# Kernel tuning notes

Hardware: AMD Instinct MI355X
Metric: run time of the kernel (lower is better)

Reference implementation:

```python
import jax, jax.numpy as jnp
import numpy as np

# Algorithm constants (scaled-down but structure-identical to the source:
# original Nxy=2304, Nz=300, ItN=60, ROISize=300, NxyExt=128, BkgMean=110, SNR=200)
ItN = 2
BkgMean = 110.0
ROISize = 256
SNR = 200.0
NxyExt = 64
Nxy = 1024
Nz = 24
LO = Nxy // 2 - ROISize   # ROI start inside the padded FFT plane
HI = Nxy // 2 + ROISize   # ROI end


def setup_inputs() -> dict:
    key = jax.random.key(0)
    k1, k2, k3, k4 = jax.random.split(key, 4)
    # raw camera image; uniform in [0, 400) so that subtracting BkgMean=110 keeps signal
    imstack = jax.random.uniform(k1, (1, 1, Nxy - 2 * NxyExt, Nxy - 2 * NxyExt), dtype=jnp.float32) * 400.0
    # initial object volume estimate (the `init` ctor arg)
    init_vol = jax.random.uniform(k2, (1, Nz, 2 * ROISize, 2 * ROISize), dtype=jnp.float32)
    # learned frequency-domain PSF kernel (rand * 0.001, as in __init__)
    conv_real = jax.random.uniform(k3, (1, 1, Nxy, Nxy), dtype=jnp.float32) * 0.001
    conv_imag = jax.random.uniform(k4, (1, 1, Nxy, Nxy), dtype=jnp.float32) * 0.001
    return {"imstack": imstack, "init_vol": init_vol, "conv_real": conv_real, "conv_imag": conv_imag}


def reference(imstack, init_vol, conv_real, conv_imag):
    # Complex frequency-domain kernel; constant across iterations (the source
    # rebuilds/casts it every slice -- same math, hoisted here).
    K = (conv_real + 1j * conv_imag)[0, 0]            # [Nxy, Nxy] complex
    Ksum = jnp.sum(conv_real)

    img = jnp.maximum(imstack - BkgMean, 0.0)
    ImgExp = jnp.pad(img, ((0, 0), (0, 0), (NxyExt, NxyExt), (NxyExt, NxyExt)))  # [1,1,Nxy,Nxy]

    obj = init_vol                                     # [1, Nz, 2R, 2R]
    for _ in range(ItN):
        # --- forward projection: batched over all Nz slices (source loops) ---
        # each slice is placed into the center ROI of a zero [Nxy,Nxy] plane
        vol = jnp.pad(obj, ((0, 0), (0, 0), (LO, Nxy - HI), (LO, Nxy - HI)))  # [1,Nz,Nxy,Nxy]
        est = jnp.real(jnp.fft.ifft2(jnp.fft.fft2(vol) * K)) / Ksum
        ImgEst = jnp.sum(jnp.maximum(est, 0.0), axis=1, keepdims=True)        # [1,1,Nxy,Nxy]

        # --- ratio image (interior only; border stays 1) ---
        Tmp = jnp.median(ImgEst)
        inner = ImgExp[:, :, NxyExt:-NxyExt, NxyExt:-NxyExt] / (
            ImgEst[:, :, NxyExt:-NxyExt, NxyExt:-NxyExt] + Tmp / SNR)
        Ratio = jnp.ones((1, 1, Nxy, Nxy), dtype=ImgEst.dtype)
        Ratio = Ratio.at[:, :, NxyExt:-NxyExt, NxyExt:-NxyExt].set(inner)

        # --- back projection: in the source, fft2(Ratio)*conj(K) is identical for
        # every jj (Ratio and K do not change inside the loop), so compute once ---
        back = jnp.real(jnp.fft.ifft2(jnp.fft.fft2(Ratio) * jnp.conj(K))) / Ksum
        back = jnp.maximum(back, 0.0)                  # [1,1,Nxy,Nxy]
        obj = obj * back[:, :, LO:HI, LO:HI]           # broadcast over Nz
    return obj
```

## Files before the change

kernel.cpp:

```cpp
#include <hip/hip_runtime.h>
#include <math.h>

#define NXY  1024
#define NZ   24
#define ROI2 512
#define LO_  256
#define EXT  64
#define IMGW 896
#define ITN  2
#define SNR_ 200.0f
#define BKG  110.0f
#define RANK1 524287u
#define RANK2 524288u
#define NACC 4
#define LSWZ(i) ((i) ^ (((i) >> 4) & 15))

typedef float2 cf;

__device__ __forceinline__ cf cadd(cf a, cf b) { return make_float2(a.x + b.x, a.y + b.y); }
__device__ __forceinline__ cf csub(cf a, cf b) { return make_float2(a.x - b.x, a.y - b.y); }
__device__ __forceinline__ cf cmul(cf a, cf b) { return make_float2(a.x * b.x - a.y * b.y, a.x * b.y + a.y * b.x); }

template <int SIGN>
__device__ __forceinline__ cf wc(float cr, float ci) { return make_float2(cr, SIGN < 0 ? ci : -ci); }

template <int SIGN>
__device__ __forceinline__ void dft4r(cf& a0, cf& a1, cf& a2, cf& a3) {
  cf b0 = cadd(a0, a2), b1 = csub(a0, a2);
  cf b2 = cadd(a1, a3), b3 = csub(a1, a3);
  cf jb3 = (SIGN < 0) ? make_float2(b3.y, -b3.x) : make_float2(-b3.y, b3.x);
  a0 = cadd(b0, b2); a2 = csub(b0, b2);
  a1 = cadd(b1, jb3); a3 = csub(b1, jb3);
}

template <int SIGN>
__device__ __forceinline__ void dft16r(cf* x) {
  const cf W1 = wc<SIGN>(0.92387953251f, -0.38268343236f);
  const cf W2 = wc<SIGN>(0.70710678119f, -0.70710678119f);
  const cf W3 = wc<SIGN>(0.38268343236f, -0.92387953251f);
  const cf W4 = wc<SIGN>(0.f, -1.f);
  const cf W6 = wc<SIGN>(-0.70710678119f, -0.70710678119f);
  const cf W9 = wc<SIGN>(-0.92387953251f, 0.38268343236f);
  cf t[16];
#pragma unroll
  for (int p = 0; p < 4; ++p) {
    cf a0 = x[p], a1 = x[p + 4], a2 = x[p + 8], a3 = x[p + 12];
    dft4r<SIGN>(a0, a1, a2, a3);
    if (p == 1) { a1 = cmul(a1, W1); a2 = cmul(a2, W2); a3 = cmul(a3, W3); }
    else if (p == 2) { a1 = cmul(a1, W2); a2 = cmul(a2, W4); a3 = cmul(a3, W6); }
    else if (p == 3) { a1 = cmul(a1, W3); a2 = cmul(a2, W6); a3 = cmul(a3, W9); }
    t[4 * p] = a0; t[4 * p + 1] = a1; t[4 * p + 2] = a2; t[4 * p + 3] = a3;
  }
#pragma unroll
  for (int q = 0; q < 4; ++q) {
    cf a0 = t[q], a1 = t[q + 4], a2 = t[q + 8], a3 = t[q + 12];
    dft4r<SIGN>(a0, a1, a2, a3);
    x[q] = a0; x[q + 4] = a1; x[q + 8] = a2; x[q + 12] = a3;
  }
}

__device__ __forceinline__ void twpow(cf* w, cf w1) {
  w[0] = make_float2(1.f, 0.f);
  w[1] = w1;
  w[2] = cmul(w1, w1);   w[3] = cmul(w[2], w1);
  w[4] = cmul(w[2], w[2]); w[5] = cmul(w[3], w[2]);
  w[6] = cmul(w[3], w[3]); w[7] = cmul(w[4], w[3]);
  w[8] = cmul(w[4], w[4]); w[9] = cmul(w[5], w[4]);
  w[10] = cmul(w[5], w[5]); w[11] = cmul(w[6], w[5]);
  w[12] = cmul(w[6], w[6]); w[13] = cmul(w[7], w[6]);
  w[14] = cmul(w[7], w[7]); w[15] = cmul(w[8], w[7]);
}

template <int SIGN>
__device__ void fft1024_wave(cf* r, cf* L, int lane) {
  const float TH = (SIGN < 0) ? -6.28318530717958647692f : 6.28318530717958647692f;
  cf w[16];
  float sv, cv;
  dft16r<SIGN>(r);
  sincosf(TH * (float)lane * (1.0f / 1024.0f), &sv, &cv);
  twpow(w, make_float2(cv, sv));
#pragma unroll
  for (int m = 1; m < 16; ++m) r[m] = cmul(r[m], w[m]);
#pragma unroll
  for (int m = 0; m < 16; ++m) L[LSWZ(16 * lane + m)] = r[m];
#pragma unroll
  for (int m = 0; m < 16; ++m) r[m] = L[LSWZ(lane + 64 * m)];
  dft16r<SIGN>(r);
  int p1 = lane >> 4, q1 = lane & 15;
  sincosf(TH * (float)p1 * (1.0f / 64.0f), &sv, &cv);
  twpow(w, make_float2(cv, sv));
#pragma unroll
  for (int m = 1; m < 16; ++m) r[m] = cmul(r[m], w[m]);
#pragma unroll
  for (int m = 0; m < 16; ++m) L[LSWZ(q1 + 256 * p1 + 16 * m)] = r[m];
#pragma unroll
  for (int j = 0; j < 16; ++j) r[j] = L[LSWZ(lane + 64 * j)];
#pragma unroll
  for (int a = 0; a < 4; ++a) dft4r<SIGN>(r[a], r[a + 4], r[a + 8], r[a + 12]);
}

__global__ void ksum_kernel(const float* __restrict__ a, float* __restrict__ out) {
  __shared__ float s[256];
  int tid = threadIdx.x;
  float acc = 0.f;
  for (int i = blockIdx.x * 256 + tid; i < NXY * NXY; i += gridDim.x * 256) acc += a[i];
  s[tid] = acc;
  __syncthreads();
  for (int o = 128; o > 0; o >>= 1) {
    if (tid < o) s[tid] += s[tid + o];
    __syncthreads();
  }
  if (tid == 0) atomicAdd(out, s[0]);
}

__global__ void imgexp_kernel(const float* __restrict__ im, float* __restrict__ out) {
  int idx = blockIdx.x * 256 + threadIdx.x;
  int r = idx >> 10, c = idx & 1023;
  float v = 0.f;
  if (r >= EXT && r < NXY - EXT && c >= EXT && c < NXY - EXT) {
    float t = im[(size_t)(r - EXT) * IMGW + (c - EXT)] - BKG;
    v = t > 0.f ? t : 0.f;
  }
  out[idx] = v;
}

__global__ void buildkh_kernel(const float* __restrict__ kre, const float* __restrict__ kim,
                               cf* __restrict__ kt) {
  int idx = blockIdx.x * 256 + threadIdx.x;
  if (idx >= 513 * 1024) return;
  int ky = idx & 1023, kx = idx >> 10;
  int ny = (1024 - ky) & 1023, nx = (1024 - kx) & 1023;
  float ar = kre[(size_t)ky * NXY + kx], ai = kim[(size_t)ky * NXY + kx];
  float br = kre[(size_t)ny * NXY + nx], bi = kim[(size_t)ny * NXY + nx];
  kt[idx] = make_float2(0.5f * (ar + br), 0.5f * (ai - bi));
}

#define S1 262144
#define S2 524288

__global__ __launch_bounds__(256) void pass1_kernel(const float* __restrict__ in, cf* __restrict__ out) {
  __shared__ cf B[4096];
  int tid = threadIdx.x, wid = tid >> 6, lane = tid & 63;
  cf* L = B + wid * 1024;
  int B0 = blockIdx.x, z = blockIdx.y;
  int p = B0 * 4 + wid;
  const float* r0 = in + ((size_t)z * 512 + 2 * p) * 512;
  const float* r1 = r0 + 512;
  cf r[16];
#pragma unroll
  for (int m = 0; m < 16; ++m) r[m] = make_float2(0.f, 0.f);
#pragma unroll
  for (int m = 4; m < 12; ++m) {
    int idx = lane + 64 * m - 256;
    r[m] = make_float2(r0[idx], r1[idx]);
  }
  fft1024_wave<-1>(r, L, lane);
#pragma unroll
  for (int j = 0; j < 16; ++j) L[LSWZ(lane + 64 * j)] = r[j];
  cf o0v[8], o1v[8];
#pragma unroll
  for (int j = 0; j < 8; ++j) {
    int k = lane + 64 * j;
    int nk = k ? (1024 - k) : 512;
    cf c = L[LSWZ(k)], d = L[LSWZ(nk)];
    if (k == 0) { o0v[j] = make_float2(c.x, d.x); o1v[j] = make_float2(c.y, d.y); }
    else {
      o0v[j] = make_float2(0.5f * (c.x + d.x), 0.5f * (c.y - d.y));
      o1v[j] = make_float2(0.5f * (c.y + d.y), 0.5f * (d.x - c.x));
    }
  }
#pragma unroll
  for (int j = 0; j < 8; ++j) {
    int k = lane + 64 * j;
    L[k] = o0v[j];
    L[512 + k] = o1v[j];
  }
  __syncthreads();
#pragma unroll
  for (int h = 0; h < 2; ++h) {
    int kx = tid + 256 * h;
    float4* dst = (float4*)(out + (size_t)z * S1 + (size_t)kx * 512 + 8 * B0);
#pragma unroll
    for (int ii = 0; ii < 4; ++ii) {
      cf a = B[(2 * ii) * 512 + kx], b = B[(2 * ii + 1) * 512 + kx];
      dst[ii] = make_float4(a.x, a.y, b.x, b.y);
    }
  }
}

__global__ __launch_bounds__(256) void pass1b_kernel(const float* __restrict__ iexp,
                                                     const float* __restrict__ iest,
                                                     const float* __restrict__ tos,
                                                     cf* __restrict__ out) {
  __shared__ cf B[4096];
  int tid = threadIdx.x, wid = tid >> 6, lane = tid & 63;
  cf* L = B + wid * 1024;
  int B0 = blockIdx.x;
  int b = B0 * 4 + wid;
  float t = tos[0];
  int r0 = 2 * b, r1 = 2 * b + 1;
  bool in0 = (r0 >= EXT && r0 < NXY - EXT);
  bool in1 = (r1 >= EXT && r1 < NXY - EXT);
  cf r[16];
#pragma unroll
  for (int m = 0; m < 16; ++m) {
    int k = lane + 64 * m;
    bool kin = (k >= EXT && k < NXY - EXT);
    float v0 = (in0 && kin) ? iexp[(size_t)r0 * NXY + k] / (iest[(size_t)r0 * NXY + k] + t) : 1.0f;
    float v1 = (in1 && kin) ? iexp[(size_t)r1 * NXY + k] / (iest[(size_t)r1 * NXY + k] + t) : 1.0f;
    r[m] = make_float2(v0, v1);
  }
  fft1024_wave<-1>(r, L, lane);
#pragma unroll
  for (int j = 0; j < 16; ++j) L[LSWZ(lane + 64 * j)] = r[j];
  cf o0v[8], o1v[8];
#pragma unroll
  for (int j = 0; j < 8; ++j) {
    int k = lane + 64 * j;
    int nk = k ? (1024 - k) : 512;
    cf c = L[LSWZ(k)], d = L[LSWZ(nk)];
    if (k == 0) { o0v[j] = make_float2(c.x, d.x); o1v[j] = make_float2(c.y, d.y); }
    else {
      o0v[j] = make_float2(0.5f * (c.x + d.x), 0.5f * (c.y - d.y));
      o1v[j] = make_float2(0.5f * (c.y + d.y), 0.5f * (d.x - c.x));
    }
  }
#pragma unroll
  for (int j = 0; j < 8; ++j) {
    int k = lane + 64 * j;
    L[k] = o0v[j];
    L[512 + k] = o1v[j];
  }
  __syncthreads();
#pragma unroll
  for (int h = 0; h < 2; ++h) {
    int kx = tid + 256 * h;
    float4* dst = (float4*)(out + (size_t)kx * NXY + 8 * B0);
#pragma unroll
    for (int ii = 0; ii < 4; ++ii) {
      cf a = B[(2 * ii) * 512 + kx], b = B[(2 * ii + 1) * 512 + kx];
      dst[ii] = make_float4(a.x, a.y, b.x, b.y);
    }
  }
}

template <int HALFIN>
__global__ __launch_bounds__(256) void pass2_kernel(const cf* __restrict__ in,
                                                    const cf* __restrict__ kt, cf* __restrict__ out,
                                                    int conjK) {
  __shared__ cf Lb[4][1024];
  int tid = threadIdx.x, wid = tid >> 6, lane = tid & 63;
  cf* L = Lb[wid];
  int kc = blockIdx.x * 4 + wid, z = blockIdx.y;
  cf kva[16];
#pragma unroll
  for (int j = 0; j < 16; ++j) {
    kva[j] = kt[(size_t)kc * NXY + lane + 64 * j];
    if (conjK) kva[j].y = -kva[j].y;
  }
  const int inLen = HALFIN ? 512 : 1024;
  const cf* src = in + ((size_t)z * 512 + kc) * inLen;
  cf r[16];
  if (HALFIN) {
#pragma unroll
    for (int m = 0; m < 16; ++m) r[m] = make_float2(0.f, 0.f);
#pragma unroll
    for (int m = 4; m < 12; ++m) r[m] = src[lane + 64 * m - 256];
  } else {
#pragma unroll
    for (int m = 0; m < 16; ++m) r[m] = src[lane + 64 * m];
  }
  fft1024_wave<-1>(r, L, lane);
  if (kc == 0) {
#pragma unroll
    for (int j = 0; j < 16; ++j) L[LSWZ(lane + 64 * j)] = r[j];
#pragma unroll
    for (int j = 0; j < 16; ++j) {
      int k = lane + 64 * j;
      int nk = (1024 - k) & 1023;
      cf c = L[LSWZ(k)], d = L[LSWZ(nk)];
      cf Fa = make_float2(0.5f * (c.x + d.x), 0.5f * (c.y - d.y));
      cf Fb = make_float2(0.5f * (c.y + d.y), 0.5f * (d.x - c.x));
      cf kb = kt[(size_t)512 * NXY + k];
      if (conjK) kb.y = -kb.y;
      cf Ga = cmul(Fa, kva[j]);
      cf Gb = cmul(Fb, kb);
      r[j] = make_float2(Ga.x - Gb.y, Ga.y + Gb.x);
    }
  } else {
#pragma unroll
    for (int j = 0; j < 16; ++j) r[j] = cmul(r[j], kva[j]);
  }
  fft1024_wave<1>(r, L, lane);
  cf* dst = out + ((size_t)z * 512 + kc) * NXY;
#pragma unroll
  for (int j = 0; j < 16; ++j) dst[lane + 64 * j] = r[j];
}

__global__ __launch_bounds__(256) void pass3_fwd_kernel(const cf* __restrict__ in,
                                                        float* __restrict__ partials,
                                                        const float* __restrict__ ksump, int zn,
                                                        int accum) {
  __shared__ cf B[4096];
  int tid = threadIdx.x, wid = tid >> 6, lane = tid & 63;
  cf* L = B + wid * 1024;
  int B0 = blockIdx.x, a = blockIdx.y;
  int y0 = 8 * B0;
  float scale = 1.0f / (1048576.0f * ksump[0]);
  cf acc[16];
#pragma unroll
  for (int j = 0; j < 16; ++j) acc[j] = make_float2(0.f, 0.f);
  cf r[16];
  for (int z = a; z < zn; z += NACC) {
    if (z != a) __syncthreads();
#pragma unroll
    for (int h = 0; h < 2; ++h) {
      int kx = tid + 256 * h;
      const float4* src = (const float4*)(in + (size_t)z * S2 + (size_t)kx * NXY + y0);
      float4 g0 = src[0], g1 = src[1], g2 = src[2], g3 = src[3];
      B[0 * 512 + kx] = make_float2(g0.x, g0.y);
      B[1 * 512 + kx] = make_float2(g0.z, g0.w);
      B[2 * 512 + kx] = make_float2(g1.x, g1.y);
      B[3 * 512 + kx] = make_float2(g1.z, g1.w);
      B[4 * 512 + kx] = make_float2(g2.x, g2.y);
      B[5 * 512 + kx] = make_float2(g2.z, g2.w);
      B[6 * 512 + kx] = make_float2(g3.x, g3.y);
      B[7 * 512 + kx] = make_float2(g3.z, g3.w);
    }
    __syncthreads();
    cf u0[8], u1[8];
#pragma unroll
    for (int j = 0; j < 8; ++j) {
      int k = lane + 64 * j;
      u0[j] = L[k];
      u1[j] = L[512 + k];
    }
#pragma unroll
    for (int j = 0; j < 8; ++j) {
      int k = lane + 64 * j;
      if (k == 0) {
        L[LSWZ(0)]   = make_float2(u0[j].x, u1[j].x);
        L[LSWZ(512)] = make_float2(u0[j].y, u1[j].y);
      } else {
        L[LSWZ(k)]        = make_float2(u0[j].x - u1[j].y, u0[j].y + u1[j].x);
        L[LSWZ(1024 - k)] = make_float2(u0[j].x + u1[j].y, u1[j].x - u0[j].y);
      }
    }
#pragma unroll
    for (int m = 0; m < 16; ++m) r[m] = L[LSWZ(lane + 64 * m)];
    fft1024_wave<1>(r, L, lane);
#pragma unroll
    for (int j = 0; j < 16; ++j) {
      float v0 = r[j].x * scale, v1 = r[j].y * scale;
      acc[j].x += v0 > 0.f ? v0 : 0.f;
      acc[j].y += v1 > 0.f ? v1 : 0.f;
    }
  }
  int r0g = y0 + 2 * wid, r1g = r0g + 1;
  float* d0 = partials + ((size_t)a * NXY + r0g) * NXY;
  float* d1 = d0 + NXY;
  if (accum) {
#pragma unroll
    for (int j = 0; j < 16; ++j) { d0[lane + 64 * j] += acc[j].x; d1[lane + 64 * j] += acc[j].y; }
  } else {
#pragma unroll
    for (int j = 0; j < 16; ++j) { d0[lane + 64 * j] = acc[j].x; d1[lane + 64 * j] = acc[j].y; }
  }
}

__global__ void fold_kernel(const float* __restrict__ partials, float* __restrict__ iest,
                            unsigned* __restrict__ st) {
  int i = blockIdx.x * 256 + threadIdx.x;
  float s = 0.f;
#pragma unroll
  for (int a = 0; a < NACC; ++a) s += partials[(size_t)a * NXY * NXY + i];
  iest[i] = s;
  if (i == 0) { st[0] = 0u; st[1] = 0u; st[2] = RANK1; st[3] = RANK2; }
}

__global__ __launch_bounds__(256) void pass3_back_kernel(const cf* __restrict__ in,
                                                         float* __restrict__ back,
                                                         const float* __restrict__ ksump) {
  __shared__ cf B[4096];
  int tid = threadIdx.x, wid = tid >> 6, lane = tid & 63;
  cf* L = B + wid * 1024;
  int B0 = blockIdx.x;
  int y0 = LO_ + 8 * B0;
  float scale = 1.0f / (1048576.0f * ksump[0]);
#pragma unroll
  for (int h = 0; h < 2; ++h) {
    int kx = tid + 256 * h;
    const float4* src = (const float4*)(in + (size_t)kx * NXY + y0);
    float4 g0 = src[0], g1 = src[1], g2 = src[2], g3 = src[3];
    B[0 * 512 + kx] = make_float2(g0.x, g0.y);
    B[1 * 512 + kx] = make_float2(g0.z, g0.w);
    B[2 * 512 + kx] = make_float2(g1.x, g1.y);
    B[3 * 512 + kx] = make_float2(g1.z, g1.w);
    B[4 * 512 + kx] = make_float2(g2.x, g2.y);
    B[5 * 512 + kx] = make_float2(g2.z, g2.w);
    B[6 * 512 + kx] = make_float2(g3.x, g3.y);
    B[7 * 512 + kx] = make_float2(g3.z, g3.w);
  }
  __syncthreads();
  cf u0[8], u1[8];
#pragma unroll
  for (int j = 0; j < 8; ++j) {
    int k = lane + 64 * j;
    u0[j] = L[k];
    u1[j] = L[512 + k];
  }
#pragma unroll
  for (int j = 0; j < 8; ++j) {
    int k = lane + 64 * j;
    if (k == 0) {
      L[LSWZ(0)]   = make_float2(u0[j].x, u1[j].x);
      L[LSWZ(512)] = make_float2(u0[j].y, u1[j].y);
    } else {
      L[LSWZ(k)]        = make_float2(u0[j].x - u1[j].y, u0[j].y + u1[j].x);
      L[LSWZ(1024 - k)] = make_float2(u0[j].x + u1[j].y, u1[j].x - u0[j].y);
    }
  }
  cf r[16];
#pragma unroll
  for (int m = 0; m < 16; ++m) r[m] = L[LSWZ(lane + 64 * m)];
  fft1024_wave<1>(r, L, lane);
  int rp0 = 8 * B0 + 2 * wid, rp1 = rp0 + 1;
#pragma unroll
  for (int j = 4; j < 12; ++j) {
    int c = lane + 64 * j - 256;
    float v0 = r[j].x * scale, v1 = r[j].y * scale;
    back[(size_t)rp0 * 512 + c] = v0 > 0.f ? v0 : 0.f;
    back[(size_t)rp1 * 512 + c] = v1 > 0.f ? v1 : 0.f;
  }
}

__global__ void mult_kernel(float* __restrict__ obj, const float* __restrict__ back) {
  int i = blockIdx.x * 256 + threadIdx.x;
  int rc4 = i & 65535;
  float4 b = ((const float4*)back)[rc4];
  float4 o = ((float4*)obj)[i];
  o.x *= b.x; o.y *= b.y; o.z *= b.z; o.w *= b.w;
  ((float4*)obj)[i] = o;
}

__global__ void medhist_kernel(const float* __restrict__ v, unsigned* __restrict__ st,
                               unsigned* __restrict__ hist, int shift, unsigned maskHigh, int nb,
                               int finalRound, float* __restrict__ tos) {
  extern __shared__ unsigned h[];
  __shared__ unsigned ps[256];
  __shared__ int lastFlag;
  int tid = threadIdx.x;
  for (int k = tid; k < 2 * nb; k += 256) h[k] = 0u;
  __syncthreads();
  unsigned p1 = st[0], p2 = st[1];
  unsigned bm = (unsigned)(nb - 1);
  for (int i = blockIdx.x * 256 + tid; i < NXY * NXY; i += gridDim.x * 256) {
    unsigned u = __float_as_uint(v[i]);
    unsigned b = (u >> shift) & bm;
    if ((u & maskHigh) == (p1 & maskHigh)) atomicAdd(&h[b], 1u);
    if ((u & maskHigh) == (p2 & maskHigh)) atomicAdd(&h[nb + b], 1u);
  }
  __syncthreads();
  for (int k = tid; k < 2 * nb; k += 256) atomicAdd(&hist[k], h[k]);
  __syncthreads();
  if (tid == 0) {
    __threadfence();
    lastFlag = (atomicAdd(&hist[4096], 1u) == (unsigned)(gridDim.x - 1)) ? 1 : 0;
  }
  __syncthreads();
  if (!lastFlag) return;
  int per = nb >> 8;
  for (int which = 0; which < 2; ++which) {
    unsigned loc[8];
    unsigned my = 0;
    for (int i = 0; i < per; ++i) { loc[i] = atomicAdd(&hist[which * nb + tid * per + i], 0u); my += loc[i]; }
    ps[tid] = my;
    __syncthreads();
    for (int off = 1; off < 256; off <<= 1) {
      unsigned vv = (tid >= off) ? ps[tid - off] : 0u;
      __syncthreads();
      ps[tid] += vv;
      __syncthreads();
    }
    unsigned pre = ps[tid] - my;
    unsigned rr = st[2 + which];
    if (rr >= pre && rr < pre + my) {
      unsigned cum = pre;
      for (int i = 0; i < per; ++i) {
        if (rr < cum + loc[i]) {
          st[which] |= (unsigned)(tid * per + i) << shift;
          st[2 + which] = rr - cum;
          break;
        }
        cum += loc[i];
      }
    }
    __syncthreads();
  }
  if (finalRound && tid == 0) {
    float m = 0.5f * (__uint_as_float(st[0]) + __uint_as_float(st[1]));
    tos[0] = m / SNR_;
  }
}

extern "C" void kernel_launch(void* const* d_in, const int* in_sizes, int n_in,
                              void* d_out, int out_size, void* d_ws, size_t ws_size,
                              hipStream_t stream) {
  const float* imstack  = (const float*)d_in[0];
  const float* init_vol = (const float*)d_in[1];
  const float* conv_re  = (const float*)d_in[2];
  const float* conv_im  = (const float*)d_in[3];
  float* obj = (float*)d_out;

  char* w = (char*)d_ws;
  size_t off = 0;
  auto alloc = [&](size_t bytes) -> void* {
    void* p = (void*)(w + off);
    off += (bytes + 255) & ~(size_t)255;
    return p;
  };

  const size_t PLANE = (size_t)NXY * NXY;
  cf* KT         = (cf*)alloc((size_t)513 * NXY * sizeof(cf));
  float* IExp    = (float*)alloc(PLANE * 4);
  float* IEst    = (float*)alloc(PLANE * 4);
  float* Partial = (float*)alloc((size_t)NACC * PLANE * 4);
  float* Back    = (float*)alloc((size_t)512 * 512 * 4);
  float* Ksum    = (float*)alloc(256);
  unsigned* St   = (unsigned*)alloc(256);
  unsigned* Hist = (unsigned*)alloc(3 * 4160 * 4);
  size_t fixedEnd = off;

  int ZC = 2;
  const int zcs[7] = {24, 12, 8, 6, 4, 3, 2};
  for (int i = 0; i < 7; ++i) {
    size_t need = fixedEnd + (size_t)zcs[i] * (S1 + S2) * sizeof(cf) + 4096;
    if (need <= ws_size) { ZC = zcs[i]; break; }
  }
  cf* bufC = (cf*)alloc((size_t)ZC * S1 * sizeof(cf));
  cf* bufD = (cf*)alloc((size_t)ZC * S2 * sizeof(cf));
  float* Tos = Ksum + 1;

  hipMemcpyAsync(obj, init_vol, (size_t)NZ * ROI2 * ROI2 * 4, hipMemcpyDeviceToDevice, stream);
  hipMemsetAsync(Ksum, 0, 8, stream);
  ksum_kernel<<<256, 256, 0, stream>>>(conv_re, Ksum);
  imgexp_kernel<<<4096, 256, 0, stream>>>(imstack, IExp);
  buildkh_kernel<<<2052, 256, 0, stream>>>(conv_re, conv_im, KT);

  const int shifts[3] = {21, 10, 0};
  const int nbs[3]    = {2048, 2048, 1024};
  const unsigned masks[3] = {0u, 0xFFE00000u, 0xFFFFFC00u};

  for (int it = 0; it < ITN; ++it) {
    for (int z0 = 0; z0 < NZ; z0 += ZC) {
      int zn = (NZ - z0 < ZC) ? (NZ - z0) : ZC;
      pass1_kernel<<<dim3(64, zn), 256, 0, stream>>>(obj + (size_t)z0 * ROI2 * ROI2, bufC);
      pass2_kernel<1><<<dim3(128, zn), 256, 0, stream>>>(bufC, KT, bufD, 0);
      pass3_fwd_kernel<<<dim3(128, NACC), 256, 0, stream>>>(bufD, Partial, Ksum, zn, z0 > 0 ? 1 : 0);
    }
    fold_kernel<<<4096, 256, 0, stream>>>(Partial, IEst, St);
    hipMemsetAsync(Hist, 0, 3 * 4160 * 4, stream);
    for (int round = 0; round < 3; ++round) {
      medhist_kernel<<<256, 256, 2 * nbs[round] * 4, stream>>>(IEst, St, Hist + round * 4160,
                                                               shifts[round], masks[round], nbs[round],
                                                               round == 2 ? 1 : 0, Tos);
    }
    pass1b_kernel<<<128, 256, 0, stream>>>(IExp, IEst, Tos, bufC);
    pass2_kernel<0><<<dim3(128, 1), 256, 0, stream>>>(bufC, KT, bufD, 1);
    pass3_back_kernel<<<64, 256, 0, stream>>>(bufD, Back, Ksum);
    mult_kernel<<<6144, 256, 0, stream>>>(obj, Back);
  }
}
```

Baseline: 590.5 us.

## Transpose pass2 output in shared memory so pass3 reads contiguous rows

```diff
diff --git a/kernel.cpp b/kernel.cpp
--- a/kernel.cpp
+++ b/kernel.cpp
@@ -12,7 +12,6 @@
 #define BKG  110.0f
 #define RANK1 524287u
 #define RANK2 524288u
-#define NACC 4
 #define LSWZ(i) ((i) ^ (((i) >> 4) & 15))
 
 typedef float2 cf;
@@ -245,13 +244,13 @@
 }
 
 template <int HALFIN>
-__global__ __launch_bounds__(256) void pass2_kernel(const cf* __restrict__ in,
-                                                    const cf* __restrict__ kt, cf* __restrict__ out,
-                                                    int conjK) {
-  __shared__ cf Lb[4][1024];
+__global__ __launch_bounds__(512, 4) void pass2_kernel(const cf* __restrict__ in,
+                                                       const cf* __restrict__ kt, cf* __restrict__ out,
+                                                       int conjK) {
+  __shared__ cf B[8192];
   int tid = threadIdx.x, wid = tid >> 6, lane = tid & 63;
-  cf* L = Lb[wid];
-  int kc = blockIdx.x * 4 + wid, z = blockIdx.y;
+  cf* L = B + wid * 1024;
+  int kc = blockIdx.x * 8 + wid, z = blockIdx.y;
   cf kva[16];
 #pragma unroll
   for (int j = 0; j < 16; ++j) {
@@ -292,9 +291,21 @@
     for (int j = 0; j < 16; ++j) r[j] = cmul(r[j], kva[j]);
   }
   fft1024_wave<1>(r, L, lane);
-  cf* dst = out + ((size_t)z * 512 + kc) * NXY;
-#pragma unroll
-  for (int j = 0; j < 16; ++j) dst[lane + 64 * j] = r[j];
+  __syncthreads();
+#pragma unroll
+  for (int j = 0; j < 16; ++j) L[lane + 64 * j] = r[j];
+  __syncthreads();
+  cf* base = out + (size_t)z * S2 + 8 * blockIdx.x;
+#pragma unroll
+  for (int h = 0; h < 2; ++h) {
+    int y = tid + 512 * h;
+    cf v[8];
+#pragma unroll
+    for (int q = 0; q < 8; ++q) v[q] = B[q * 1024 + y];
+    float4* dst = (float4*)(base + (size_t)y * 512);
+#pragma unroll
+    for (int q = 0; q < 4; ++q) dst[q] = make_float4(v[2 * q].x, v[2 * q].y, v[2 * q + 1].x, v[2 * q + 1].y);
+  }
 }
 
 __global__ __launch_bounds__(256) void pass3_fwd_kernel(const cf* __restrict__ in,
@@ -304,46 +315,27 @@
   __shared__ cf B[4096];
   int tid = threadIdx.x, wid = tid >> 6, lane = tid & 63;
   cf* L = B + wid * 1024;
-  int B0 = blockIdx.x, a = blockIdx.y;
-  int y0 = 8 * B0;
+  int p = blockIdx.x * 4 + wid, a = blockIdx.y;
+  int nacc = gridDim.y;
+  int r0 = 2 * p, r1 = 2 * p + 1;
   float scale = 1.0f / (1048576.0f * ksump[0]);
   cf acc[16];
 #pragma unroll
   for (int j = 0; j < 16; ++j) acc[j] = make_float2(0.f, 0.f);
   cf r[16];
-  for (int z = a; z < zn; z += NACC) {
-    if (z != a) __syncthreads();
-#pragma unroll
-    for (int h = 0; h < 2; ++h) {
-      int kx = tid + 256 * h;
-      const float4* src = (const float4*)(in + (size_t)z * S2 + (size_t)kx * NXY + y0);
-      float4 g0 = src[0], g1 = src[1], g2 = src[2], g3 = src[3];
-      B[0 * 512 + kx] = make_float2(g0.x, g0.y);
-      B[1 * 512 + kx] = make_float2(g0.z, g0.w);
-      B[2 * 512 + kx] = make_float2(g1.x, g1.y);
-      B[3 * 512 + kx] = make_float2(g1.z, g1.w);
-      B[4 * 512 + kx] = make_float2(g2.x, g2.y);
-      B[5 * 512 + kx] = make_float2(g2.z, g2.w);
-      B[6 * 512 + kx] = make_float2(g3.x, g3.y);
-      B[7 * 512 + kx] = make_float2(g3.z, g3.w);
-    }
-    __syncthreads();
-    cf u0[8], u1[8];
+  for (int z = a; z < zn; z += nacc) {
+    const cf* s0 = in + (size_t)z * S2 + (size_t)r0 * 512;
+    const cf* s1 = s0 + 512;
 #pragma unroll
     for (int j = 0; j < 8; ++j) {
       int k = lane + 64 * j;
-      u0[j] = L[k];
-      u1[j] = L[512 + k];
-    }
-#pragma unroll
-    for (int j = 0; j < 8; ++j) {
-      int k = lane + 64 * j;
+      cf u0 = s0[k], u1 = s1[k];
       if (k == 0) {
-        L[LSWZ(0)]   = make_float2(u0[j].x, u1[j].x);
-        L[LSWZ(512)] = make_float2(u0[j].y, u1[j].y);
+        L[LSWZ(0)]   = make_float2(u0.x, u1.x);
+        L[LSWZ(512)] = make_float2(u0.y, u1.y);
       } else {
-        L[LSWZ(k)]        = make_float2(u0[j].x - u1[j].y, u0[j].y + u1[j].x);
-        L[LSWZ(1024 - k)] = make_float2(u0[j].x + u1[j].y, u1[j].x - u0[j].y);
+        L[LSWZ(k)]        = make_float2(u0.x - u1.y, u0.y + u1.x);
+        L[LSWZ(1024 - k)] = make_float2(u0.x + u1.y, u1.x - u0.y);
       }
     }
 #pragma unroll
@@ -356,8 +348,7 @@
       acc[j].y += v1 > 0.f ? v1 : 0.f;
     }
   }
-  int r0g = y0 + 2 * wid, r1g = r0g + 1;
-  float* d0 = partials + ((size_t)a * NXY + r0g) * NXY;
+  float* d0 = partials + ((size_t)a * NXY + r0) * NXY;
   float* d1 = d0 + NXY;
   if (accum) {
 #pragma unroll
@@ -369,11 +360,10 @@
 }
 
 __global__ void fold_kernel(const float* __restrict__ partials, float* __restrict__ iest,
-                            unsigned* __restrict__ st) {
+                            unsigned* __restrict__ st, int nacc) {
   int i = blockIdx.x * 256 + threadIdx.x;
   float s = 0.f;
-#pragma unroll
-  for (int a = 0; a < NACC; ++a) s += partials[(size_t)a * NXY * NXY + i];
+  for (int a = 0; a < nacc; ++a) s += partials[(size_t)a * NXY * NXY + i];
   iest[i] = s;
   if (i == 0) { st[0] = 0u; st[1] = 0u; st[2] = RANK1; st[3] = RANK2; }
 }
@@ -384,47 +374,28 @@
   __shared__ cf B[4096];
   int tid = threadIdx.x, wid = tid >> 6, lane = tid & 63;
   cf* L = B + wid * 1024;
-  int B0 = blockIdx.x;
-  int y0 = LO_ + 8 * B0;
+  int p = blockIdx.x * 4 + wid;
   float scale = 1.0f / (1048576.0f * ksump[0]);
-#pragma unroll
-  for (int h = 0; h < 2; ++h) {
-    int kx = tid + 256 * h;
-    const float4* src = (const float4*)(in + (size_t)kx * NXY + y0);
-    float4 g0 = src[0], g1 = src[1], g2 = src[2], g3 = src[3];
-    B[0 * 512 + kx] = make_float2(g0.x, g0.y);
-    B[1 * 512 + kx] = make_float2(g0.z, g0.w);
-    B[2 * 512 + kx] = make_float2(g1.x, g1.y);
-    B[3 * 512 + kx] = make_float2(g1.z, g1.w);
-    B[4 * 512 + kx] = make_float2(g2.x, g2.y);
-    B[5 * 512 + kx] = make_float2(g2.z, g2.w);
-    B[6 * 512 + kx] = make_float2(g3.x, g3.y);
-    B[7 * 512 + kx] = make_float2(g3.z, g3.w);
-  }
-  __syncthreads();
-  cf u0[8], u1[8];
+  int r0 = LO_ + 2 * p, r1 = r0 + 1;
+  const cf* s0 = in + (size_t)r0 * 512;
+  const cf* s1 = in + (size_t)r1 * 512;
 #pragma unroll
   for (int j = 0; j < 8; ++j) {
     int k = lane + 64 * j;
-    u0[j] = L[k];
-    u1[j] = L[512 + k];
-  }
-#pragma unroll
-  for (int j = 0; j < 8; ++j) {
-    int k = lane + 64 * j;
+    cf u0 = s0[k], u1 = s1[k];
     if (k == 0) {
-      L[LSWZ(0)]   = make_float2(u0[j].x, u1[j].x);
-      L[LSWZ(512)] = make_float2(u0[j].y, u1[j].y);
+      L[LSWZ(0)]   = make_float2(u0.x, u1.x);
+      L[LSWZ(512)] = make_float2(u0.y, u1.y);
     } else {
-      L[LSWZ(k)]        = make_float2(u0[j].x - u1[j].y, u0[j].y + u1[j].x);
-      L[LSWZ(1024 - k)] = make_float2(u0[j].x + u1[j].y, u1[j].x - u0[j].y);
+      L[LSWZ(k)]        = make_float2(u0.x - u1.y, u0.y + u1.x);
+      L[LSWZ(1024 - k)] = make_float2(u0.x + u1.y, u1.x - u0.y);
     }
   }
   cf r[16];
 #pragma unroll
   for (int m = 0; m < 16; ++m) r[m] = L[LSWZ(lane + 64 * m)];
   fft1024_wave<1>(r, L, lane);
-  int rp0 = 8 * B0 + 2 * wid, rp1 = rp0 + 1;
+  int rp0 = 2 * p, rp1 = rp0 + 1;
 #pragma unroll
   for (int j = 4; j < 12; ++j) {
     int c = lane + 64 * j - 256;
@@ -524,19 +495,25 @@
   cf* KT         = (cf*)alloc((size_t)513 * NXY * sizeof(cf));
   float* IExp    = (float*)alloc(PLANE * 4);
   float* IEst    = (float*)alloc(PLANE * 4);
-  float* Partial = (float*)alloc((size_t)NACC * PLANE * 4);
   float* Back    = (float*)alloc((size_t)512 * 512 * 4);
   float* Ksum    = (float*)alloc(256);
   unsigned* St   = (unsigned*)alloc(256);
   unsigned* Hist = (unsigned*)alloc(3 * 4160 * 4);
   size_t fixedEnd = off;
 
-  int ZC = 2;
-  const int zcs[7] = {24, 12, 8, 6, 4, 3, 2};
-  for (int i = 0; i < 7; ++i) {
-    size_t need = fixedEnd + (size_t)zcs[i] * (S1 + S2) * sizeof(cf) + 4096;
-    if (need <= ws_size) { ZC = zcs[i]; break; }
-  }
+  int ZC = 2, NACC = 4;
+  {
+    const int zcs[7] = {24, 12, 8, 6, 4, 3, 2};
+    const int nas[2] = {8, 4};
+    bool done = false;
+    for (int i = 0; i < 7 && !done; ++i)
+      for (int j = 0; j < 2 && !done; ++j) {
+        size_t need = fixedEnd + (size_t)nas[j] * PLANE * 4 +
+                      (size_t)zcs[i] * (S1 + S2) * sizeof(cf) + 8192;
+        if (need <= ws_size) { ZC = zcs[i]; NACC = nas[j]; done = true; }
+      }
+  }
+  float* Partial = (float*)alloc((size_t)NACC * PLANE * 4);
   cf* bufC = (cf*)alloc((size_t)ZC * S1 * sizeof(cf));
   cf* bufD = (cf*)alloc((size_t)ZC * S2 * sizeof(cf));
   float* Tos = Ksum + 1;
@@ -555,10 +532,10 @@
     for (int z0 = 0; z0 < NZ; z0 += ZC) {
       int zn = (NZ - z0 < ZC) ? (NZ - z0) : ZC;
       pass1_kernel<<<dim3(64, zn), 256, 0, stream>>>(obj + (size_t)z0 * ROI2 * ROI2, bufC);
-      pass2_kernel<1><<<dim3(128, zn), 256, 0, stream>>>(bufC, KT, bufD, 0);
+      pass2_kernel<1><<<dim3(64, zn), 512, 0, stream>>>(bufC, KT, bufD, 0);
       pass3_fwd_kernel<<<dim3(128, NACC), 256, 0, stream>>>(bufD, Partial, Ksum, zn, z0 > 0 ? 1 : 0);
     }
-    fold_kernel<<<4096, 256, 0, stream>>>(Partial, IEst, St);
+    fold_kernel<<<4096, 256, 0, stream>>>(Partial, IEst, St, NACC);
     hipMemsetAsync(Hist, 0, 3 * 4160 * 4, stream);
     for (int round = 0; round < 3; ++round) {
       medhist_kernel<<<256, 256, 2 * nbs[round] * 4, stream>>>(IEst, St, Hist + round * 4160,
@@ -566,7 +543,7 @@
                                                                round == 2 ? 1 : 0, Tos);
     }
     pass1b_kernel<<<128, 256, 0, stream>>>(IExp, IEst, Tos, bufC);
-    pass2_kernel<0><<<dim3(128, 1), 256, 0, stream>>>(bufC, KT, bufD, 1);
+    pass2_kernel<0><<<dim3(64, 1), 512, 0, stream>>>(bufC, KT, bufD, 1);
     pass3_back_kernel<<<64, 256, 0, stream>>>(bufD, Back, Ksum);
     mult_kernel<<<6144, 256, 0, stream>>>(obj, Back);
   }
```

Measured after the change: 859.6 us. 1.46x slower.
